# Kernel tuning notes

Hardware: AMD Instinct MI355X
Metric: run time of the kernel (lower is better)

## Reference

```python
import jax, jax.numpy as jnp
import numpy as np

T, B, D = 1024, 32, 1024


def setup_inputs() -> dict:
    key = jax.random.key(0)
    k_x, k_wa, k_wh, k_wx = jax.random.split(key, 4)
    s = 1.0 / np.sqrt(D)  # xavier-ish scale
    x = jax.random.normal(k_x, (T, B, D), dtype=jnp.float32)
    h0 = jnp.zeros((B, D), dtype=jnp.float32)
    W_alpha = jax.random.normal(k_wa, (D, D), dtype=jnp.float32) * s
    b_alpha = jnp.full((D,), 2.0, dtype=jnp.float32)  # init_alpha_bias = 2.0
    W_h = jax.random.normal(k_wh, (D, D), dtype=jnp.float32) * (0.5 * s)  # orthogonal*0.5 approx
    W_x = jax.random.normal(k_wx, (D, D), dtype=jnp.float32) * s
    b = jnp.zeros((D,), dtype=jnp.float32)
    return {"x": x, "h0": h0, "W_alpha": W_alpha, "b_alpha": b_alpha,
            "W_h": W_h, "W_x": W_x, "b": b}


def reference(x, h0, W_alpha, b_alpha, W_h, W_x, b):
    # Precompute input-dependent terms (batched over T*B)
    alpha_all = jax.nn.sigmoid(jnp.einsum('tbd,ed->tbe', x, W_alpha) + b_alpha)  # [T,B,D]
    Wx_all = jnp.einsum('tbd,ed->tbe', x, W_x) + b                               # [T,B,D]

    def step(h_prev, inp):
        alpha, wx = inp
        v = jnp.tanh(h_prev @ W_h.T + wx)            # nonlinear in h
        h_new = alpha * h_prev + (1.0 - alpha) * v   # complementary gate
        out = h_new * jax.nn.silu(h_new)
        return h_new, (out, h_new)

    _, (output, hs) = jax.lax.scan(step, h0, (alpha_all, Wx_all))
    h = jnp.concatenate([h0[None], hs], axis=0)  # [T+1, B, D]
    return output, h
```

## Files before the change

### kernel.cpp

```cpp
#include <hip/hip_runtime.h>
#include <hip/hip_bf16.h>
#include <stdint.h>

#define TT 1024
#define BB 32
#define DD 1024

typedef __attribute__((ext_vector_type(8))) short short8;
typedef __attribute__((ext_vector_type(4))) unsigned short ushort4v;
typedef __attribute__((ext_vector_type(4))) float floatx4;
typedef __attribute__((ext_vector_type(4))) unsigned uint4v;

static __device__ __forceinline__ unsigned short f2bf(float f){
  unsigned u = __float_as_uint(f);
  u += 0x7fffu + ((u >> 16) & 1u);
  return (unsigned short)(u >> 16);
}
static __device__ __forceinline__ float bf2f(unsigned short s){
  return __uint_as_float(((unsigned)s) << 16);
}
static __device__ __forceinline__ float sigm(float x){
  return __fdividef(1.0f, 1.0f + __expf(-x));
}
static __device__ __forceinline__ float fast_tanh(float x){
  float e = __expf(2.0f * x);
  return 1.0f - __fdividef(2.0f, e + 1.0f);
}

#define WS_FRAG_BYTES (134217728ull)
#define WS_WCAT_OFF   (WS_FRAG_BYTES)
#define WS_WCAT_BYTES (4194304ull)
#define WS_H0T_OFF    (WS_WCAT_OFF + WS_WCAT_BYTES)
#define WS_H1T_OFF    (WS_H0T_OFF + 131072ull)

__global__ void init_kernel(const float* __restrict__ Wa, const float* __restrict__ Wx,
                            const float* __restrict__ h0, float* __restrict__ hout0,
                            unsigned short* __restrict__ Wcat,
                            unsigned long long* __restrict__ h0T,
                            unsigned long long* __restrict__ h1T)
{
  long i = (long)blockIdx.x * 256 + threadIdx.x;
  const long NW = 2048L * 1024L;
  for (long idx = i; idx < NW; idx += (long)gridDim.x * 256L){
    long r = idx >> 10, c = idx & 1023;
    float v = (r < 1024) ? Wa[r*1024 + c] : Wx[(r-1024)*1024 + c];
    Wcat[idx] = f2bf(v);
  }
  const long NG = 32L * 512L;
  for (long idx = i; idx < NG; idx += (long)gridDim.x * 256L){
    long row = idx >> 9, cp = idx & 511;
    float a = h0[row*1024 + 2*cp], b = h0[row*1024 + 2*cp + 1];
    unsigned hpair = ((unsigned)f2bf(b) << 16) | (unsigned)f2bf(a);
    h0T[idx] = ((unsigned long long)0x00010001u << 32) | hpair;
    h1T[idx] = 0ull;
  }
  const long NH = 32L * 1024L;
  for (long idx = i; idx < NH; idx += (long)gridDim.x * 256L)
    hout0[idx] = h0[idx];
}

__global__ __launch_bounds__(256) void pre_gemm(
    const float* __restrict__ x, const unsigned short* __restrict__ Wcat,
    const float* __restrict__ b_alpha, const float* __restrict__ b_x,
    unsigned short* __restrict__ frag)
{
  __shared__ unsigned short A_lds[128*72];
  __shared__ unsigned short B_lds[128*72];
  const int tid = threadIdx.x;
  const int lane = tid & 63;
  const int w = tid >> 6;
  const int wm = w >> 1, wn = w & 1;
  const long m0 = (long)blockIdx.y * 128;
  const int n0 = blockIdx.x * 128;

  floatx4 acc[4][4];
#pragma unroll
  for (int i=0;i<4;++i)
#pragma unroll
    for (int j=0;j<4;++j) acc[i][j] = (floatx4){0.f,0.f,0.f,0.f};

  for (int kt=0; kt<16; ++kt){
    const int k0 = kt*64;
    __syncthreads();
#pragma unroll
    for (int rep=0; rep<4; ++rep){
      int flat = rep*2048 + tid*8;
      int r = flat >> 6, c = flat & 63;
      const float* src = &x[(m0 + r)*1024 + k0 + c];
      floatx4 f0 = *(const floatx4*)src;
      floatx4 f1 = *(const floatx4*)(src + 4);
      short8 v;
      v[0]=(short)f2bf(f0[0]); v[1]=(short)f2bf(f0[1]); v[2]=(short)f2bf(f0[2]); v[3]=(short)f2bf(f0[3]);
      v[4]=(short)f2bf(f1[0]); v[5]=(short)f2bf(f1[1]); v[6]=(short)f2bf(f1[2]); v[7]=(short)f2bf(f1[3]);
      *(short8*)&A_lds[r*72 + c] = v;
      short8 bv = *(const short8*)&Wcat[(long)(n0 + r)*1024 + k0 + c];
      *(short8*)&B_lds[r*72 + c] = bv;
    }
    __syncthreads();
#pragma unroll
    for (int kb=0; kb<2; ++kb){
      short8 a[4], b[4];
#pragma unroll
      for (int f=0; f<4; ++f)
        a[f] = *(const short8*)&A_lds[(wm*64 + f*16 + (lane&15))*72 + kb*32 + (lane>>4)*8];
#pragma unroll
      for (int f=0; f<4; ++f)
        b[f] = *(const short8*)&B_lds[(wn*64 + f*16 + (lane&15))*72 + kb*32 + (lane>>4)*8];
#pragma unroll
      for (int fm=0; fm<4; ++fm)
#pragma unroll
        for (int fn=0; fn<4; ++fn)
          acc[fm][fn] = __builtin_amdgcn_mfma_f32_16x16x32_bf16(a[fm], b[fn], acc[fm][fn], 0, 0, 0);
    }
  }

#pragma unroll
  for (int fm=0; fm<4; ++fm){
    const long mrow = m0 + wm*64 + fm*16;
    const int t  = (int)(mrow >> 5);
    const int bh = (int)((mrow >> 4) & 1);
#pragma unroll
    for (int fn=0; fn<4; ++fn){
      const int nf  = n0 + wn*64 + fn*16;
      const int nt  = nf >> 4;
      const int col = nf + (lane & 15);
      floatx4 v = acc[fm][fn];
      const float bias = (col < DD) ? b_alpha[col] : b_x[col - DD];
      ushort4v o;
#pragma unroll
      for (int i=0;i<4;++i) o[i] = f2bf(v[i] + bias);
      *(ushort4v*)&frag[((((long)t*2 + bh)*128 + nt)*64 + lane)*4] = o;
    }
  }
}

__global__ __launch_bounds__(256, 1) void scan_kernel(
    const float* __restrict__ Wh, const float* __restrict__ h0,
    unsigned short* frag,
    unsigned long long* h0T,
    unsigned long long* h1T)
{
  __shared__ unsigned h_lds[16*512];
  const int tid  = threadIdx.x;
  const int lane = tid & 63;
  const int w    = tid >> 6;
  const int bh   = blockIdx.x & 1;
  const int s    = blockIdx.x >> 1;
  const int base_r = s * 64;

  const int g8   = (lane >> 4) * 8;
  const int brow = w*16 + (lane & 15);

  short8 Breg[32];
  {
    const float* Wr = &Wh[(long)(base_r + brow)*1024 + g8];
#pragma unroll
    for (int kb=0; kb<32; ++kb){
      floatx4 f0 = *(const floatx4*)&Wr[kb*32];
      floatx4 f1 = *(const floatx4*)&Wr[kb*32 + 4];
      short8 v;
      v[0]=(short)f2bf(f0[0]); v[1]=(short)f2bf(f0[1]); v[2]=(short)f2bf(f0[2]); v[3]=(short)f2bf(f0[3]);
      v[4]=(short)f2bf(f1[0]); v[5]=(short)f2bf(f1[1]); v[6]=(short)f2bf(f1[2]); v[7]=(short)f2bf(f1[3]);
      Breg[kb] = v;
    }
  }

  const int colf = base_r + w*16 + (lane & 15);
  const int nt_a = (base_r + w*16) >> 4;
  float hp[4];
#pragma unroll
  for (int i=0;i<4;++i){
    int gb = bh*16 + (lane>>4)*4 + i;
    hp[i] = h0[(long)gb*1024 + colf];
  }

  const int rowq = w*4 + (lane>>4);
  const int cpl  = lane & 15;
  const int row_a = lane & 15;
  const int rsw_w = (rowq & 7) << 2;
  const int rsw_r = (row_a & 7) << 2;

  long fb = (((long)0*2 + bh)*128 + nt_a)*64 + lane;
  ushort4v al = *(const ushort4v*)&frag[fb*4];
  ushort4v wx = *(const ushort4v*)&frag[(fb + 64*64)*4];

  const int ceven = colf & ~1;
  const bool iseven = ((lane & 1) == 0);

  for (int t=0; t<TT; ++t){
    const unsigned long long* hU =
        (t == 0) ? (h0T + bh*8192) :
        (t == 1) ? (h1T + bh*8192) :
                   (const unsigned long long*)(frag + ((long)(t-2)*2 + bh)*32768);
    const unsigned tt = ((unsigned)(t+1) << 16) | (unsigned)(t+1);

    unsigned long long d[32];
    for (;;){
#pragma unroll
      for (int j=0; j<32; ++j)
        d[j] = __hip_atomic_load(&hU[rowq*512 + cpl + 16*j],
                                 __ATOMIC_RELAXED, __HIP_MEMORY_SCOPE_AGENT);
      unsigned bad = 0;
#pragma unroll
      for (int j=0; j<32; ++j)
        bad |= ((unsigned)(d[j] >> 32)) ^ tt;
      if (__all(bad == 0)) break;
    }

#pragma unroll
    for (int j=0; j<32; ++j){
      const int cp = cpl + 16*j;
      h_lds[rowq*512 + (((cp & ~3) ^ rsw_w) | (cp & 3))] = (unsigned)d[j];
    }
    __syncthreads();

    floatx4 ac0 = (floatx4){0.f,0.f,0.f,0.f}, ac1 = ac0, ac2 = ac0, ac3 = ac0;
#pragma unroll
    for (int kb=0; kb<32; ++kb){
      uint4v q = *(const uint4v*)&h_lds[row_a*512 + ((kb*16 + (g8>>1)) ^ rsw_r)];
      short8 afr = __builtin_bit_cast(short8, q);
      if ((kb&3)==0) ac0 = __builtin_amdgcn_mfma_f32_16x16x32_bf16(afr, Breg[kb], ac0, 0, 0, 0);
      if ((kb&3)==1) ac1 = __builtin_amdgcn_mfma_f32_16x16x32_bf16(afr, Breg[kb], ac1, 0, 0, 0);
      if ((kb&3)==2) ac2 = __builtin_amdgcn_mfma_f32_16x16x32_bf16(afr, Breg[kb], ac2, 0, 0, 0);
      if ((kb&3)==3) ac3 = __builtin_amdgcn_mfma_f32_16x16x32_bf16(afr, Breg[kb], ac3, 0, 0, 0);
    }
    floatx4 acc = (ac0 + ac1) + (ac2 + ac3);
    __syncthreads();

    unsigned long long* hD =
        (t == 0) ? (h1T + bh*8192)
                 : (unsigned long long*)(frag + ((long)(t-1)*2 + bh)*32768);
    const unsigned ttn = ((unsigned)(t+2) << 16) | (unsigned)(t+2);
#pragma unroll
    for (int i=0;i<4;++i){
      float sv = acc[i] + bf2f(wx[i]);
      float v  = fast_tanh(sv);
      float aa = sigm(bf2f(al[i]));
      float hn = aa*hp[i] + (1.0f - aa)*v;
      hp[i] = hn;
      unsigned us    = (unsigned)f2bf(hn);
      unsigned other = (unsigned)__shfl_xor((int)us, 1, 64);
      if (iseven){
        unsigned hpair = (other << 16) | us;
        unsigned long long pv = ((unsigned long long)ttn << 32) | hpair;
        const int r = (lane>>4)*4 + i;
        __hip_atomic_store(&hD[r*512 + (ceven>>1)], pv,
                           __ATOMIC_RELAXED, __HIP_MEMORY_SCOPE_AGENT);
      }
    }

    if (t + 1 < TT){
      fb = (((long)(t+1)*2 + bh)*128 + nt_a)*64 + lane;
      al = *(const ushort4v*)&frag[fb*4];
      wx = *(const ushort4v*)&frag[(fb + 64*64)*4];
    }
  }
}

__global__ __launch_bounds__(256) void out_writer(
    const unsigned short* __restrict__ frag,
    const unsigned long long* __restrict__ h1T,
    float* __restrict__ out, float* __restrict__ hout)
{
  const int t1 = blockIdx.z + 1;
  const int bh = blockIdx.y;
  const int e  = (blockIdx.x*256 + threadIdx.x)*8;
  const int row = e >> 10, col = e & 1023;
  const unsigned long long* src =
      (t1 == 1) ? (h1T + bh*8192)
                : (const unsigned long long*)(frag + ((long)(t1-2)*2 + bh)*32768);
  const unsigned long long* p = &src[row*512 + (col>>1)];
  float o[8], hh[8];
#pragma unroll
  for (int g=0; g<4; ++g){
    unsigned hpair = (unsigned)p[g];
    float ha = bf2f((unsigned short)(hpair & 0xFFFFu));
    float hb = bf2f((unsigned short)(hpair >> 16));
    float sa = sigm(ha), sb = sigm(hb);
    hh[2*g] = ha;            hh[2*g+1] = hb;
    o[2*g]  = ha*ha*sa;      o[2*g+1]  = hb*hb*sb;
  }
  long ob = ((long)(t1-1)*BB + bh*16 + row)*DD + col;
  long hb = ((long)t1*BB + bh*16 + row)*DD + col;
  *(floatx4*)&out[ob]     = (floatx4){o[0],o[1],o[2],o[3]};
  *(floatx4*)&out[ob+4]   = (floatx4){o[4],o[5],o[6],o[7]};
  *(floatx4*)&hout[hb]    = (floatx4){hh[0],hh[1],hh[2],hh[3]};
  *(floatx4*)&hout[hb+4]  = (floatx4){hh[4],hh[5],hh[6],hh[7]};
}

extern "C" void kernel_launch(void* const* d_in, const int* in_sizes, int n_in,
                              void* d_out, int out_size, void* d_ws, size_t ws_size,
                              hipStream_t stream)
{
  const float* x  = (const float*)d_in[0];
  const float* h0 = (const float*)d_in[1];
  const float* Wa = (const float*)d_in[2];
  const float* ba = (const float*)d_in[3];
  const float* Wh = (const float*)d_in[4];
  const float* Wx = (const float*)d_in[5];
  const float* bx = (const float*)d_in[6];

  float* out  = (float*)d_out;
  float* hout = out + (long)TT*BB*DD;

  uint8_t* ws = (uint8_t*)d_ws;
  unsigned short*     frag = (unsigned short*)(ws);
  unsigned short*     Wcat = (unsigned short*)(ws + WS_WCAT_OFF);
  unsigned long long* h0T  = (unsigned long long*)(ws + WS_H0T_OFF);
  unsigned long long* h1T  = (unsigned long long*)(ws + WS_H1T_OFF);

  init_kernel<<<8192, 256, 0, stream>>>(Wa, Wx, h0, hout, Wcat, h0T, h1T);
  pre_gemm<<<dim3(16, 256), 256, 0, stream>>>(x, Wcat, ba, bx, frag);
  scan_kernel<<<32, 256, 0, stream>>>(Wh, h0, frag, h0T, h1T);
  out_writer<<<dim3(8, 2, 1024), 256, 0, stream>>>(frag, h1T, out, hout);
}
```

Before: 3.885 ms.

## Double-buffer LDS h tile, vectorize polling loads, drop second barrier

```diff
diff --git a/kernel.cpp b/kernel.cpp
--- a/kernel.cpp
+++ b/kernel.cpp
@@ -10,6 +10,7 @@
 typedef __attribute__((ext_vector_type(4))) unsigned short ushort4v;
 typedef __attribute__((ext_vector_type(4))) float floatx4;
 typedef __attribute__((ext_vector_type(4))) unsigned uint4v;
+typedef __attribute__((ext_vector_type(2))) unsigned uint2v;
 
 static __device__ __forceinline__ unsigned short f2bf(float f){
   unsigned u = __float_as_uint(f);
@@ -140,7 +141,7 @@
     unsigned long long* h0T,
     unsigned long long* h1T)
 {
-  __shared__ unsigned h_lds[16*512];
+  __shared__ unsigned h_lds[2][16*512];
   const int tid  = threadIdx.x;
   const int lane = tid & 63;
   const int w    = tid >> 6;
@@ -174,15 +175,19 @@
     hp[i] = h0[(long)gb*1024 + colf];
   }
 
-  const int rowq = w*4 + (lane>>4);
-  const int cpl  = lane & 15;
+  const int lrow = tid >> 4;
+  const int lc2  = (tid & 15) * 2;
+  const int swl  = (lrow & 7) ^ ((lrow & 1) << 3);
   const int row_a = lane & 15;
-  const int rsw_w = (rowq & 7) << 2;
-  const int rsw_r = (row_a & 7) << 2;
+  const int swr  = (row_a & 7) ^ ((row_a & 1) << 3);
 
   long fb = (((long)0*2 + bh)*128 + nt_a)*64 + lane;
-  ushort4v al = *(const ushort4v*)&frag[fb*4];
-  ushort4v wx = *(const ushort4v*)&frag[(fb + 64*64)*4];
+  unsigned long long a0v = __hip_atomic_load((const unsigned long long*)&frag[fb*4],
+                                             __ATOMIC_RELAXED, __HIP_MEMORY_SCOPE_AGENT);
+  unsigned long long w0v = __hip_atomic_load((const unsigned long long*)&frag[(fb + 64*64)*4],
+                                             __ATOMIC_RELAXED, __HIP_MEMORY_SCOPE_AGENT);
+  ushort4v al = __builtin_bit_cast(ushort4v, a0v);
+  ushort4v wx = __builtin_bit_cast(ushort4v, w0v);
 
   const int ceven = colf & ~1;
   const bool iseven = ((lane & 1) == 0);
@@ -193,31 +198,42 @@
         (t == 1) ? (h1T + bh*8192) :
                    (const unsigned long long*)(frag + ((long)(t-2)*2 + bh)*32768);
     const unsigned tt = ((unsigned)(t+1) << 16) | (unsigned)(t+1);
-
-    unsigned long long d[32];
-    for (;;){
-#pragma unroll
-      for (int j=0; j<32; ++j)
-        d[j] = __hip_atomic_load(&hU[rowq*512 + cpl + 16*j],
-                                 __ATOMIC_RELAXED, __HIP_MEMORY_SCOPE_AGENT);
-      unsigned bad = 0;
-#pragma unroll
-      for (int j=0; j<32; ++j)
-        bad |= ((unsigned)(d[j] >> 32)) ^ tt;
-      if (__all(bad == 0)) break;
-    }
-
-#pragma unroll
-    for (int j=0; j<32; ++j){
-      const int cp = cpl + 16*j;
-      h_lds[rowq*512 + (((cp & ~3) ^ rsw_w) | (cp & 3))] = (unsigned)d[j];
+    unsigned* HB = h_lds[t & 1];
+
+#pragma unroll
+    for (int b=0; b<2; ++b){
+      uint4v L[8];
+#pragma unroll
+      for (int j=0; j<8; ++j)
+        L[j] = *(const uint4v*)&hU[lrow*512 + lc2 + 32*(8*b + j)];
+#pragma unroll
+      for (int j=0; j<8; ++j){
+        const int cp0 = lc2 + 32*(8*b + j);
+        const int idx = lrow*512 + (((cp0 >> 2) ^ swl) << 2) + (cp0 & 3);
+        *(uint2v*)&HB[idx] = (uint2v){L[j][0], L[j][2]};
+        if (L[j][1] != tt){
+          unsigned long long g;
+          do { g = __hip_atomic_load(&hU[lrow*512 + cp0],
+                                     __ATOMIC_RELAXED, __HIP_MEMORY_SCOPE_AGENT);
+          } while ((unsigned)(g >> 32) != tt);
+          HB[idx] = (unsigned)g;
+        }
+        if (L[j][3] != tt){
+          unsigned long long g;
+          do { g = __hip_atomic_load(&hU[lrow*512 + cp0 + 1],
+                                     __ATOMIC_RELAXED, __HIP_MEMORY_SCOPE_AGENT);
+          } while ((unsigned)(g >> 32) != tt);
+          HB[idx + 1] = (unsigned)g;
+        }
+      }
     }
     __syncthreads();
 
     floatx4 ac0 = (floatx4){0.f,0.f,0.f,0.f}, ac1 = ac0, ac2 = ac0, ac3 = ac0;
 #pragma unroll
     for (int kb=0; kb<32; ++kb){
-      uint4v q = *(const uint4v*)&h_lds[row_a*512 + ((kb*16 + (g8>>1)) ^ rsw_r)];
+      const int u = kb*4 + (lane>>4);
+      uint4v q = *(const uint4v*)&HB[row_a*512 + ((u ^ swr) << 2)];
       short8 afr = __builtin_bit_cast(short8, q);
       if ((kb&3)==0) ac0 = __builtin_amdgcn_mfma_f32_16x16x32_bf16(afr, Breg[kb], ac0, 0, 0, 0);
       if ((kb&3)==1) ac1 = __builtin_amdgcn_mfma_f32_16x16x32_bf16(afr, Breg[kb], ac1, 0, 0, 0);
@@ -225,7 +241,6 @@
       if ((kb&3)==3) ac3 = __builtin_amdgcn_mfma_f32_16x16x32_bf16(afr, Breg[kb], ac3, 0, 0, 0);
     }
     floatx4 acc = (ac0 + ac1) + (ac2 + ac3);
-    __syncthreads();
 
     unsigned long long* hD =
         (t == 0) ? (h1T + bh*8192)
@@ -251,8 +266,12 @@
 
     if (t + 1 < TT){
       fb = (((long)(t+1)*2 + bh)*128 + nt_a)*64 + lane;
-      al = *(const ushort4v*)&frag[fb*4];
-      wx = *(const ushort4v*)&frag[(fb + 64*64)*4];
+      unsigned long long av = __hip_atomic_load((const unsigned long long*)&frag[fb*4],
+                                                __ATOMIC_RELAXED, __HIP_MEMORY_SCOPE_AGENT);
+      unsigned long long wv = __hip_atomic_load((const unsigned long long*)&frag[(fb + 64*64)*4],
+                                                __ATOMIC_RELAXED, __HIP_MEMORY_SCOPE_AGENT);
+      al = __builtin_bit_cast(ushort4v, av);
+      wx = __builtin_bit_cast(ushort4v, wv);
     }
   }
 }
```

Result: slower. 5.132 ms (+32.1%).
